# Performance work log

Measured on AMD Instinct MI355X. Metric: run time of the kernel, lower is better.

## Reference

```python
import jax, jax.numpy as jnp
import numpy as np
from jax import lax

B, T, D, H, L = 2048, 512, 64, 16, 10
LOG2PI = float(np.log(2.0 * np.pi))


def _gru_cell(x, h, Wih, Whh, bih, bhh):
    # torch GRUCell gate order: r, z, n
    gi = x @ Wih.T + bih
    gh = h @ Whh.T + bhh
    ir, iz, inn = jnp.split(gi, 3, axis=-1)
    hr, hz, hn = jnp.split(gh, 3, axis=-1)
    r = jax.nn.sigmoid(ir + hr)
    z = jax.nn.sigmoid(iz + hz)
    n = jnp.tanh(inn + r * hn)
    return (1.0 - z) * n + z * h


def _mlp_head(h, W1, b1, W2, b2, Wmu, bmu, Wcov, bcov):
    hh = jax.nn.relu(h @ W1.T + b1)
    hh = jax.nn.relu(hh @ W2.T + b2)
    mu = hh @ Wmu.T + bmu
    sigma = jnp.exp(hh @ Wcov.T + bcov)
    return mu, sigma


def setup_inputs():
    key = jax.random.key(0)
    ks = jax.random.split(key, 24)

    def he(k, shape, fan_in):
        return jax.random.normal(k, shape, dtype=jnp.float32) * np.float32(np.sqrt(2.0 / fan_in))

    z = lambda *s: jnp.zeros(s, jnp.float32)
    p = {}
    p['x'] = jax.random.normal(ks[0], (B, T, D), dtype=jnp.float32)
    p['eps'] = jax.random.normal(ks[1], (B, T, L), dtype=jnp.float32)
    # bidirectional inference GRU
    p['bi_Wih_f'] = he(ks[2], (3 * H, D), D); p['bi_Whh_f'] = he(ks[3], (3 * H, H), H)
    p['bi_bih_f'] = z(3 * H); p['bi_bhh_f'] = z(3 * H)
    p['bi_Wih_b'] = he(ks[4], (3 * H, D), D); p['bi_Whh_b'] = he(ks[5], (3 * H, H), H)
    p['bi_bih_b'] = z(3 * H); p['bi_bhh_b'] = z(3 * H)
    # inference GRUCell on [z_prev, context]
    p['infz_Wih'] = he(ks[6], (3 * H, L + 2 * H), L + 2 * H); p['infz_Whh'] = he(ks[7], (3 * H, H), H)
    p['infz_bih'] = z(3 * H); p['infz_bhh'] = z(3 * H)
    # inference MLP
    p['inf_W1'] = he(ks[8], (H, H), H); p['inf_b1'] = z(H)
    p['inf_W2'] = he(ks[9], (H, H), H); p['inf_b2'] = z(H)
    p['inf_Wmu'] = he(ks[10], (L, H), H); p['inf_bmu'] = z(L)
    p['inf_Wcov'] = he(ks[11], (L, H), H); p['inf_bcov'] = z(L)
    # generative prior GRUCell + MLP (frozen in torch)
    p['genz_Wih'] = he(ks[12], (3 * H, L), L); p['genz_Whh'] = he(ks[13], (3 * H, H), H)
    p['genz_bih'] = z(3 * H); p['genz_bhh'] = z(3 * H)
    p['genzmlp_W1'] = he(ks[14], (H, H), H); p['genzmlp_b1'] = z(H)
    p['genzmlp_W2'] = he(ks[15], (H, H), H); p['genzmlp_b2'] = z(H)
    p['genzmlp_Wmu'] = he(ks[16], (L, H), H); p['genzmlp_bmu'] = z(L)
    p['genzmlp_Wcov'] = he(ks[17], (L, H), H); p['genzmlp_bcov'] = z(L)
    # generative emission GRUCell + MLP (outputs 3*D)
    p['genr_Wih'] = he(ks[18], (3 * H, L), L); p['genr_Whh'] = he(ks[19], (3 * H, H), H)
    p['genr_bih'] = z(3 * H); p['genr_bhh'] = z(3 * H)
    p['genr_W1'] = he(ks[20], (H, H), H); p['genr_b1'] = z(H)
    p['genr_W2'] = he(ks[21], (3 * D, H), H); p['genr_b2'] = z(3 * D)
    return p


def _forward(x, eps, bi_Wih_f, bi_Whh_f, bi_bih_f, bi_bhh_f, bi_Wih_b, bi_Whh_b, bi_bih_b, bi_bhh_b,
             infz_Wih, infz_Whh, infz_bih, infz_bhh,
             inf_W1, inf_b1, inf_W2, inf_b2, inf_Wmu, inf_bmu, inf_Wcov, inf_bcov,
             genz_Wih, genz_Whh, genz_bih, genz_bhh,
             genzmlp_W1, genzmlp_b1, genzmlp_W2, genzmlp_b2, genzmlp_Wmu, genzmlp_bmu, genzmlp_Wcov, genzmlp_bcov,
             genr_Wih, genr_Whh, genr_bih, genr_bhh, genr_W1, genr_b1, genr_W2, genr_b2):
    b, t, d = x.shape
    xt = jnp.transpose(x, (1, 0, 2))      # [T, B, D] time-major
    eps_t = jnp.transpose(eps, (1, 0, 2))  # [T, B, L]
    h0 = jnp.zeros((b, H), x.dtype)

    def fstep(h, xin):
        h2 = _gru_cell(xin, h, bi_Wih_f, bi_Whh_f, bi_bih_f, bi_bhh_f)
        return h2, h2

    def bstep(h, xin):
        h2 = _gru_cell(xin, h, bi_Wih_b, bi_Whh_b, bi_bih_b, bi_bhh_b)
        return h2, h2

    _, fwd = lax.scan(fstep, h0, xt)               # [T, B, H]
    _, bwd_rev = lax.scan(bstep, h0, xt[::-1])
    bwd = bwd_rev[::-1]                            # [T, B, H]

    pad = jnp.zeros((1, b, H), x.dtype)
    h_right = jnp.concatenate([pad, fwd[:-1]], axis=0)   # h^{->}_{t-1}
    h_left = jnp.concatenate([bwd[1:], pad], axis=0)     # h^{<-}_{t+1}
    ctx = jnp.concatenate([h_right, h_left], axis=-1)    # [T, B, 2H]

    def step(carry, inp):
        h_z, h_gz, h_gr, z_prev = carry
        c, e, xi = inp
        h_z = _gru_cell(jnp.concatenate([z_prev, c], axis=-1), h_z, infz_Wih, infz_Whh, infz_bih, infz_bhh)
        q_mu, q_sig = _mlp_head(h_z, inf_W1, inf_b1, inf_W2, inf_b2, inf_Wmu, inf_bmu, inf_Wcov, inf_bcov)
        h_gz = _gru_cell(z_prev, h_gz, genz_Wih, genz_Whh, genz_bih, genz_bhh)
        p_mu, p_sig = _mlp_head(h_gz, genzmlp_W1, genzmlp_b1, genzmlp_W2, genzmlp_b2, genzmlp_Wmu, genzmlp_bmu, genzmlp_Wcov, genzmlp_bcov)
        # KL(N(q_mu,q_sig) || N(p_mu,p_sig))
        kl = jnp.log(p_sig / q_sig) + (q_sig * q_sig + (q_mu - p_mu) ** 2) / (2.0 * p_sig * p_sig) - 0.5
        kl_t = kl.sum(axis=-1).mean()
        z_t = q_mu + q_sig * e  # rsample
        h_gr = _gru_cell(z_t, h_gr, genr_Wih, genr_Whh, genr_bih, genr_bhh)
        r = jax.nn.relu(h_gr @ genr_W1.T + genr_b1) @ genr_W2.T + genr_b2  # [B, 3D]
        r_mu = r[:, :d]
        r_diag = jnp.exp(r[:, d:2 * d]) + 1e-4
        w = r[:, 2 * d:]  # rank-1 cov factor
        # LowRankMVN log_prob via Woodbury (rank 1): Cov = D + w w^T
        delta = xi - r_mu
        dinv = 1.0 / r_diag
        wd = w * dinv
        cap = 1.0 + jnp.sum(wd * w, axis=-1)  # capacitance
        maha = jnp.sum(delta * delta * dinv, axis=-1) - jnp.sum(wd * delta, axis=-1) ** 2 / cap
        logdet = jnp.sum(jnp.log(r_diag), axis=-1) + jnp.log(cap)
        logp = -0.5 * (d * LOG2PI + logdet + maha)
        nll_t = -logp.mean()
        return (h_z, h_gz, h_gr, z_t), (kl_t, nll_t)

    z0 = jnp.zeros((b, L), x.dtype)
    carry0 = (h0, h0, h0, z0)
    _, (kls, nlls) = lax.scan(step, carry0, (ctx, eps_t, xt))
    return nlls.sum(), kls.sum()


def reference(x, eps, bi_Wih_f, bi_Whh_f, bi_bih_f, bi_bhh_f, bi_Wih_b, bi_Whh_b, bi_bih_b, bi_bhh_b,
              infz_Wih, infz_Whh, infz_bih, infz_bhh,
              inf_W1, inf_b1, inf_W2, inf_b2, inf_Wmu, inf_bmu, inf_Wcov, inf_bcov,
              genz_Wih, genz_Whh, genz_bih, genz_bhh,
              genzmlp_W1, genzmlp_b1, genzmlp_W2, genzmlp_b2, genzmlp_Wmu, genzmlp_bmu, genzmlp_Wcov, genzmlp_bcov,
              genr_Wih, genr_Whh, genr_bih, genr_bhh, genr_W1, genr_b1, genr_W2, genr_b2):
    return _forward(x, eps, bi_Wih_f, bi_Whh_f, bi_bih_f, bi_bhh_f, bi_Wih_b, bi_Whh_b, bi_bih_b, bi_bhh_b,
                    infz_Wih, infz_Whh, infz_bih, infz_bhh,
                    inf_W1, inf_b1, inf_W2, inf_b2, inf_Wmu, inf_bmu, inf_Wcov, inf_bcov,
                    genz_Wih, genz_Whh, genz_bih, genz_bhh,
                    genzmlp_W1, genzmlp_b1, genzmlp_W2, genzmlp_b2, genzmlp_Wmu, genzmlp_bmu, genzmlp_Wcov, genzmlp_bcov,
                    genr_Wih, genr_Whh, genr_bih, genr_bhh, genr_W1, genr_b1, genr_W2, genr_b2)
```

## Files before the change

### kernel.cpp

```cpp
#include <hip/hip_runtime.h>

namespace {

typedef __attribute__((ext_vector_type(4))) _Float16 half4v;
typedef __attribute__((ext_vector_type(4))) float   float4v;
typedef unsigned int u32;

#define MFMA16(a,b,c) __builtin_amdgcn_mfma_f32_16x16x16f16((a),(b),(c),0,0,0)

constexpr int Bb = 2048;
constexpr int Tt = 512;
constexpr float LOG2PI_ = 1.8378770664093453f;

struct InPtrs { const float* p[42]; };

__device__ __forceinline__ float rcpf(float x){ return __builtin_amdgcn_rcpf(x); }
__device__ __forceinline__ float sigm(float x){ return rcpf(1.0f + __expf(-x)); }
__device__ __forceinline__ float tanh_(float x){ return 1.0f - 2.0f*rcpf(1.0f + __expf(2.0f*x)); }

__device__ __forceinline__ void barrier_lds(){
  asm volatile("s_waitcnt lgkmcnt(0)" ::: "memory");
  __builtin_amdgcn_s_barrier();
  asm volatile("" ::: "memory");
}

__global__ void zero2(float* out){ if (threadIdx.x < 2) out[threadIdx.x] = 0.f; }

__device__ __forceinline__ void gru_update(const float4v& Dr, const float4v& Dz,
                                           const float4v& Dn, const float4v& Dh, half4v& hB){
  #pragma unroll
  for (int i = 0; i < 4; ++i){
    const float rr = sigm(Dr[i]);
    const float zz = sigm(Dz[i]);
    const float nn = tanh_(Dn[i] + rr*Dh[i]);
    const float hp = (float)hB[i];
    hB[i] = (_Float16)((1.f - zz)*nn + zz*hp);
  }
}

__device__ __forceinline__ half4v relu_pack(const float4v& D){
  half4v o;
  #pragma unroll
  for (int i = 0; i < 4; ++i) o[i] = (_Float16)fmaxf(D[i], 0.f);
  return o;
}

constexpr int CH = 8;
constexpr int NCH = Tt / CH;

__global__ __launch_bounds__(128,1) void bigru(InPtrs ip, _Float16* __restrict__ hf,
                                               _Float16* __restrict__ hb)
{
  const int tid = threadIdx.x;
  const int w = tid >> 6;
  const int l = tid & 63, r = l & 15, q = l >> 4;
  const int dir = blockIdx.y;
  const int base = blockIdx.x * 16;

  const float* __restrict__ x   = ip.p[0];
  const float* __restrict__ Wih = dir ? ip.p[6] : ip.p[2];
  const float* __restrict__ Whh = dir ? ip.p[7] : ip.p[3];
  const float* __restrict__ bih = dir ? ip.p[8] : ip.p[4];
  const float* __restrict__ bhh = dir ? ip.p[9] : ip.p[5];
  _Float16* __restrict__ hout = dir ? hb : hf;

  __shared__ __align__(16) float giS[2][CH][64][12];

  half4v Wi[3][4];
  float  b0[4], b1[4], b2[4];
  float4v xp[CH][4];
  half4v Wh[3];
  float  bh2[4];
  half4v hB = {0,0,0,0};
  const float* xrow = x + (size_t)(base + r) * Tt * 64;

  if (w == 1){
    #pragma unroll
    for (int rt = 0; rt < 3; ++rt)
      #pragma unroll
      for (int kt = 0; kt < 4; ++kt)
        #pragma unroll
        for (int j = 0; j < 4; ++j)
          Wi[rt][kt][j] = (_Float16)Wih[(rt*16 + r)*64 + kt*16 + q*4 + j];
    #pragma unroll
    for (int i = 0; i < 4; ++i){
      const int row = q*4 + i;
      b0[i] = bih[row]      + bhh[row];
      b1[i] = bih[16 + row] + bhh[16 + row];
      b2[i] = bih[32 + row];
    }
    #pragma unroll
    for (int s = 0; s < CH; ++s){
      const int tn = dir ? Tt-1-s : s;
      #pragma unroll
      for (int kt = 0; kt < 4; ++kt)
        xp[s][kt] = *(const float4v*)(xrow + (size_t)tn*64 + kt*16 + q*4);
    }
  } else {
    #pragma unroll
    for (int rt = 0; rt < 3; ++rt)
      #pragma unroll
      for (int j = 0; j < 4; ++j)
        Wh[rt][j] = (_Float16)Whh[(rt*16 + r)*16 + q*4 + j];
    #pragma unroll
    for (int i = 0; i < 4; ++i) bh2[i] = bhh[32 + q*4 + i];
  }

  for (int c = 0; c < NCH; ++c){
    if (w == 1){
      #pragma unroll
      for (int st = 0; st < CH; ++st){
        const int tg = c*CH + st;
        half4v xB[4];
        #pragma unroll
        for (int kt = 0; kt < 4; ++kt)
          #pragma unroll
          for (int j = 0; j < 4; ++j) xB[kt][j] = (_Float16)xp[st][kt][j];
        const int tp = tg + CH;
        if (tp < Tt){
          const int tn = dir ? Tt-1-tp : tp;
          #pragma unroll
          for (int kt = 0; kt < 4; ++kt)
            xp[st][kt] = *(const float4v*)(xrow + (size_t)tn*64 + kt*16 + q*4);
        }
        float4v A0 = {b0[0],b0[1],b0[2],b0[3]};
        float4v A1 = {b1[0],b1[1],b1[2],b1[3]};
        float4v A2 = {b2[0],b2[1],b2[2],b2[3]};
        #pragma unroll
        for (int kt = 0; kt < 4; ++kt){
          A0 = MFMA16(Wi[0][kt], xB[kt], A0);
          A1 = MFMA16(Wi[1][kt], xB[kt], A1);
          A2 = MFMA16(Wi[2][kt], xB[kt], A2);
        }
        float* o = &giS[c&1][st][l][0];
        *(float4v*)(o + 0) = A0;
        *(float4v*)(o + 4) = A1;
        *(float4v*)(o + 8) = A2;
      }
    }
    barrier_lds();
    if (w == 0){
      for (int st = 0; st < CH; ++st){
        const int tg = c*CH + st;
        const int t = dir ? Tt-1-tg : tg;
        const float* gi = &giS[c&1][st][l][0];
        float4v A0 = *(const float4v*)(gi + 0);
        float4v A1 = *(const float4v*)(gi + 4);
        float4v A2 = *(const float4v*)(gi + 8);
        float4v Dh = {bh2[0],bh2[1],bh2[2],bh2[3]};
        A0 = MFMA16(Wh[0], hB, A0);
        A1 = MFMA16(Wh[1], hB, A1);
        Dh = MFMA16(Wh[2], hB, Dh);
        gru_update(A0, A1, A2, Dh, hB);
        *(half4v*)(hout + (((size_t)t*Bb + base + r) << 4) + q*4) = hB;
      }
    }
  }
}

__global__ __launch_bounds__(192,1) void vae_seq(InPtrs ip, const _Float16* __restrict__ hf,
                                                 const _Float16* __restrict__ hb,
                                                 _Float16* __restrict__ hz,
                                                 _Float16* __restrict__ hgz,
                                                 _Float16* __restrict__ hgr)
{
  const int tid = threadIdx.x;
  const int w = tid / 64;
  const int l = tid & 63, r = l & 15, q = l >> 4;
  const int base = blockIdx.x * 16;
  const int row0 = q*4;

  __shared__ u32 zS[3][2][64];
  for (int i = tid; i < 3*2*64; i += 192) ((u32*)zS)[i] = 0u;
  barrier_lds();

  half4v WizA[3][3], WhzA[3], I1A, I2A, IMuA, ICovA;
  float bz0[4], bz1[4], bzn[4], bzh[4], bI1v[4], bI2v[4], bIMu[4], bICov[4];
  half4v hzB = {0,0,0,0}, zB = {0,0,0,0};
  half4v hrN = {0,0,0,0}, hlN = {0,0,0,0};
  float eN[4];
  half4v WgzA[3], WhgzA[3];
  float bg0[4], bg1[4], bgn[4], bgh[4];
  half4v hgzB = {0,0,0,0};
  half4v WgrA[3], WhgrA[3];
  float br0[4], br1[4], brn[4], brh[4];
  half4v hgrB = {0,0,0,0};

  const float* erow = ip.p[1] + (size_t)(base + r) * Tt * 10;

  if (w == 0){
    #pragma unroll
    for (int rt = 0; rt < 3; ++rt)
      #pragma unroll
      for (int kt = 0; kt < 3; ++kt)
        #pragma unroll
        for (int j = 0; j < 4; ++j){
          const int k = kt*16 + q*4 + j;
          int c;
          if (kt == 0) c = (k < 10) ? k : -1;
          else if (kt == 1) c = 10 + (k - 16);
          else c = 26 + (k - 32);
          WizA[rt][kt][j] = (c >= 0) ? (_Float16)ip.p[10][(rt*16 + r)*42 + c] : (_Float16)0.f;
        }
    #pragma unroll
    for (int rt = 0; rt < 3; ++rt)
      #pragma unroll
      for (int j = 0; j < 4; ++j)
        WhzA[rt][j] = (_Float16)ip.p[11][(rt*16 + r)*16 + q*4 + j];
    #pragma unroll
    for (int j = 0; j < 4; ++j){
      const int k = q*4 + j;
      I1A[j]  = (_Float16)ip.p[14][r*16 + k];
      I2A[j]  = (_Float16)ip.p[16][r*16 + k];
      IMuA[j] = (r < 10) ? (_Float16)ip.p[18][r*16 + k] : (_Float16)0.f;
      ICovA[j]= (r < 10) ? (_Float16)ip.p[20][r*16 + k] : (_Float16)0.f;
    }
    #pragma unroll
    for (int i = 0; i < 4; ++i){
      const int row = row0 + i;
      bz0[i] = ip.p[12][row]    + ip.p[13][row];
      bz1[i] = ip.p[12][16+row] + ip.p[13][16+row];
      bzn[i] = ip.p[12][32+row];
      bzh[i] = ip.p[13][32+row];
      bI1v[i] = ip.p[15][row];  bI2v[i] = ip.p[17][row];
      bIMu[i]  = (row < 10) ? ip.p[19][row] : 0.f;
      bICov[i] = (row < 10) ? ip.p[21][row] : 0.f;
    }
    hlN = *(const half4v*)(hb + (((size_t)1*Bb + base + r) << 4) + q*4);
    #pragma unroll
    for (int i = 0; i < 4; ++i) eN[i] = (row0 + i < 10) ? erow[row0 + i] : 0.f;
  } else if (w == 1){
    #pragma unroll
    for (int rt = 0; rt < 3; ++rt)
      #pragma unroll
      for (int j = 0; j < 4; ++j){
        const int k = q*4 + j;
        WgzA[rt][j]  = (k < 10) ? (_Float16)ip.p[22][(rt*16 + r)*10 + k] : (_Float16)0.f;
        WhgzA[rt][j] = (_Float16)ip.p[23][(rt*16 + r)*16 + k];
      }
    #pragma unroll
    for (int i = 0; i < 4; ++i){
      const int row = row0 + i;
      bg0[i] = ip.p[24][row]    + ip.p[25][row];
      bg1[i] = ip.p[24][16+row] + ip.p[25][16+row];
      bgn[i] = ip.p[24][32+row];
      bgh[i] = ip.p[25][32+row];
    }
  } else {
    #pragma unroll
    for (int rt = 0; rt < 3; ++rt)
      #pragma unroll
      for (int j = 0; j < 4; ++j){
        const int k = q*4 + j;
        WgrA[rt][j]  = (k < 10) ? (_Float16)ip.p[34][(rt*16 + r)*10 + k] : (_Float16)0.f;
        WhgrA[rt][j] = (_Float16)ip.p[35][(rt*16 + r)*16 + k];
      }
    #pragma unroll
    for (int i = 0; i < 4; ++i){
      const int row = row0 + i;
      br0[i] = ip.p[36][row]    + ip.p[37][row];
      br1[i] = ip.p[36][16+row] + ip.p[37][16+row];
      brn[i] = ip.p[36][32+row];
      brh[i] = ip.p[37][32+row];
    }
  }

  for (int i = 0; i < Tt + 2; ++i){
    if (w == 0){
      if (i < Tt){
        const half4v hrB = hrN, hlB = hlN;
        float ev[4];
        #pragma unroll
        for (int ii = 0; ii < 4; ++ii) ev[ii] = eN[ii];
        if (i < Tt-1){
          const int tn = i + 1;
          hrN = *(const half4v*)(hf + (((size_t)(tn-1)*Bb + base + r) << 4) + q*4);
          if (tn < Tt-1) hlN = *(const half4v*)(hb + (((size_t)(tn+1)*Bb + base + r) << 4) + q*4);
          else { half4v zz0 = {0,0,0,0}; hlN = zz0; }
          #pragma unroll
          for (int ii = 0; ii < 4; ++ii) eN[ii] = (row0 + ii < 10) ? erow[tn*10 + row0 + ii] : 0.f;
        }
        float4v Dr = {bz0[0],bz0[1],bz0[2],bz0[3]};
        float4v Dz = {bz1[0],bz1[1],bz1[2],bz1[3]};
        float4v Dn = {bzn[0],bzn[1],bzn[2],bzn[3]};
        float4v Dh = {bzh[0],bzh[1],bzh[2],bzh[3]};
        Dr = MFMA16(WizA[0][0], zB, Dr); Dr = MFMA16(WizA[0][1], hrB, Dr); Dr = MFMA16(WizA[0][2], hlB, Dr);
        Dz = MFMA16(WizA[1][0], zB, Dz); Dz = MFMA16(WizA[1][1], hrB, Dz); Dz = MFMA16(WizA[1][2], hlB, Dz);
        Dn = MFMA16(WizA[2][0], zB, Dn); Dn = MFMA16(WizA[2][1], hrB, Dn); Dn = MFMA16(WizA[2][2], hlB, Dn);
        Dr = MFMA16(WhzA[0], hzB, Dr);
        Dz = MFMA16(WhzA[1], hzB, Dz);
        Dh = MFMA16(WhzA[2], hzB, Dh);
        gru_update(Dr, Dz, Dn, Dh, hzB);
        *(half4v*)(hz + (((size_t)i*Bb + base + r) << 4) + q*4) = hzB;

        float4v H1 = {bI1v[0],bI1v[1],bI1v[2],bI1v[3]};
        H1 = MFMA16(I1A, hzB, H1);
        const half4v h1B = relu_pack(H1);
        float4v H2 = {bI2v[0],bI2v[1],bI2v[2],bI2v[3]};
        H2 = MFMA16(I2A, h1B, H2);
        const half4v h2B = relu_pack(H2);
        float4v Qmu  = {bIMu[0],bIMu[1],bIMu[2],bIMu[3]};
        float4v Qpre = {bICov[0],bICov[1],bICov[2],bICov[3]};
        Qmu  = MFMA16(IMuA,  h2B, Qmu);
        Qpre = MFMA16(ICovA, h2B, Qpre);

        const int slot = i % 3;
        #pragma unroll
        for (int ii = 0; ii < 4; ++ii){
          const float qs = __expf(Qpre[ii]);
          zB[ii] = (_Float16)(Qmu[ii] + qs*ev[ii]);
        }
        union { half4v h; u32 u[2]; } zc; zc.h = zB;
        zS[slot][0][l] = zc.u[0];
        zS[slot][1][l] = zc.u[1];
      }
    } else if (w == 1){
      if (i >= 1 && i <= Tt){
        const int s = i - 1;
        const int sp = (s - 1 + 3) % 3;
        union { half4v h; u32 u[2]; } zc;
        zc.u[0] = zS[sp][0][l]; zc.u[1] = zS[sp][1][l];
        const half4v zPrev = zc.h;

        float4v Er = {bg0[0],bg0[1],bg0[2],bg0[3]};
        float4v Ez = {bg1[0],bg1[1],bg1[2],bg1[3]};
        float4v En = {bgn[0],bgn[1],bgn[2],bgn[3]};
        float4v Eh = {bgh[0],bgh[1],bgh[2],bgh[3]};
        Er = MFMA16(WgzA[0], zPrev, Er); Er = MFMA16(WhgzA[0], hgzB, Er);
        Ez = MFMA16(WgzA[1], zPrev, Ez); Ez = MFMA16(WhgzA[1], hgzB, Ez);
        En = MFMA16(WgzA[2], zPrev, En);
        Eh = MFMA16(WhgzA[2], hgzB, Eh);
        gru_update(Er, Ez, En, Eh, hgzB);
        *(half4v*)(hgz + (((size_t)s*Bb + base + r) << 4) + q*4) = hgzB;
      }
    } else {
      if (i >= 2){
        const int u = i - 2;
        union { half4v h; u32 uu[2]; } zc;
        zc.uu[0] = zS[u % 3][0][l]; zc.uu[1] = zS[u % 3][1][l];
        const half4v zU = zc.h;

        float4v Fr = {br0[0],br0[1],br0[2],br0[3]};
        float4v Fz = {br1[0],br1[1],br1[2],br1[3]};
        float4v Fn = {brn[0],brn[1],brn[2],brn[3]};
        float4v Fh = {brh[0],brh[1],brh[2],brh[3]};
        Fr = MFMA16(WgrA[0], zU, Fr); Fr = MFMA16(WhgrA[0], hgrB, Fr);
        Fz = MFMA16(WgrA[1], zU, Fz); Fz = MFMA16(WhgrA[1], hgrB, Fz);
        Fn = MFMA16(WgrA[2], zU, Fn);
        Fh = MFMA16(WhgrA[2], hgrB, Fh);
        gru_update(Fr, Fz, Fn, Fh, hgrB);
        *(half4v*)(hgr + (((size_t)u*Bb + base + r) << 4) + q*4) = hgrB;
      }
    }
    barrier_lds();
  }
}

__global__ __launch_bounds__(256,4) void kl_epi(InPtrs ip, const _Float16* __restrict__ hz,
                                                const _Float16* __restrict__ hgz,
                                                float* __restrict__ out)
{
  const int tid = threadIdx.x;
  const int l = tid & 63, r = l & 15, q = l >> 4;
  const int row0 = q*4;
  const int wid = blockIdx.x * 4 + (tid >> 6);
  const int u0 = wid * 16;

  half4v I1A, I2A, IMuA, ICovA, Z1A, Z2A, ZMuA, ZCovA;
  float bI1v[4], bI2v[4], bIMu[4], bICov[4], bZ1v[4], bZ2v[4], bZMu[4], bZCov[4];
  #pragma unroll
  for (int j = 0; j < 4; ++j){
    const int k = q*4 + j;
    I1A[j]  = (_Float16)ip.p[14][r*16 + k];
    I2A[j]  = (_Float16)ip.p[16][r*16 + k];
    IMuA[j] = (r < 10) ? (_Float16)ip.p[18][r*16 + k] : (_Float16)0.f;
    ICovA[j]= (r < 10) ? (_Float16)ip.p[20][r*16 + k] : (_Float16)0.f;
    Z1A[j]  = (_Float16)ip.p[26][r*16 + k];
    Z2A[j]  = (_Float16)ip.p[28][r*16 + k];
    ZMuA[j] = (r < 10) ? (_Float16)ip.p[30][r*16 + k] : (_Float16)0.f;
    ZCovA[j]= (r < 10) ? (_Float16)ip.p[32][r*16 + k] : (_Float16)0.f;
  }
  #pragma unroll
  for (int i = 0; i < 4; ++i){
    const int row = row0 + i;
    bI1v[i] = ip.p[15][row];  bI2v[i] = ip.p[17][row];
    bIMu[i]  = (row < 10) ? ip.p[19][row] : 0.f;
    bICov[i] = (row < 10) ? ip.p[21][row] : 0.f;
    bZ1v[i] = ip.p[27][row];  bZ2v[i] = ip.p[29][row];
    bZMu[i]  = (row < 10) ? ip.p[31][row] : 0.f;
    bZCov[i] = (row < 10) ? ip.p[33][row] : 0.f;
  }

  float kl_acc = 0.f;
  for (int k = 0; k < 16; ++k){
    const int u = u0 + k;
    const int tile = u >> 9, t = u & 511;
    const size_t off = (((size_t)t*Bb + tile*16 + r) << 4) + q*4;
    const half4v hzB  = *(const half4v*)(hz  + off);
    const half4v hgzB = *(const half4v*)(hgz + off);

    float4v H1 = {bI1v[0],bI1v[1],bI1v[2],bI1v[3]};
    H1 = MFMA16(I1A, hzB, H1);
    const half4v h1B = relu_pack(H1);
    float4v H2 = {bI2v[0],bI2v[1],bI2v[2],bI2v[3]};
    H2 = MFMA16(I2A, h1B, H2);
    const half4v h2B = relu_pack(H2);
    float4v Qmu  = {bIMu[0],bIMu[1],bIMu[2],bIMu[3]};
    float4v Qpre = {bICov[0],bICov[1],bICov[2],bICov[3]};
    Qmu  = MFMA16(IMuA,  h2B, Qmu);
    Qpre = MFMA16(ICovA, h2B, Qpre);

    float4v G1 = {bZ1v[0],bZ1v[1],bZ1v[2],bZ1v[3]};
    G1 = MFMA16(Z1A, hgzB, G1);
    const half4v g1B = relu_pack(G1);
    float4v G2 = {bZ2v[0],bZ2v[1],bZ2v[2],bZ2v[3]};
    G2 = MFMA16(Z2A, g1B, G2);
    const half4v g2B = relu_pack(G2);
    float4v Pmu  = {bZMu[0],bZMu[1],bZMu[2],bZMu[3]};
    float4v Ppre = {bZCov[0],bZCov[1],bZCov[2],bZCov[3]};
    Pmu  = MFMA16(ZMuA,  g2B, Pmu);
    Ppre = MFMA16(ZCovA, g2B, Ppre);

    #pragma unroll
    for (int ii = 0; ii < 4; ++ii){
      const float qs = __expf(Qpre[ii]);
      const float dm = Qmu[ii] - Pmu[ii];
      kl_acc += (Ppre[ii] - Qpre[ii]) + (qs*qs + dm*dm)*0.5f*__expf(-2.f*Ppre[ii]) - 0.5f;
    }
  }
  #pragma unroll
  for (int m = 1; m < 64; m <<= 1) kl_acc += __shfl_xor(kl_acc, m, 64);
  if (l == 0) atomicAdd(&out[1], kl_acc * (1.f/(float)Bb));
}

__global__ __launch_bounds__(256,2) void nll_epi(InPtrs ip, const _Float16* __restrict__ hgr,
                                                 float* __restrict__ out)
{
  const int tid = threadIdx.x;
  const int l = tid & 63, r = l & 15, q = l >> 4;
  const int row0 = q*4;
  const int wid = blockIdx.x * 4 + (tid >> 6);
  const int u0 = wid * 16;

  half4v R1A, R2A[12];
  float bR1v[4], bR2v[12][4];
  #pragma unroll
  for (int j = 0; j < 4; ++j){
    const int k = q*4 + j;
    R1A[j] = (_Float16)ip.p[38][r*16 + k];
    #pragma unroll
    for (int m = 0; m < 12; ++m)
      R2A[m][j] = (_Float16)ip.p[40][(m*16 + r)*16 + k];
  }
  #pragma unroll
  for (int i = 0; i < 4; ++i){
    const int row = row0 + i;
    bR1v[i] = ip.p[39][row];
    #pragma unroll
    for (int m = 0; m < 12; ++m) bR2v[m][i] = ip.p[41][m*16 + row];
  }

  float nll_acc = 0.f;
  for (int k = 0; k < 16; ++k){
    const int u = u0 + k;
    const int tile = u >> 9, t = u & 511;
    const half4v hgrB = *(const half4v*)(hgr + (((size_t)t*Bb + tile*16 + r) << 4) + q*4);
    const float* xrow = ip.p[0] + ((size_t)(tile*16 + r) * Tt + t) * 64;
    float4v xv[4];
    #pragma unroll
    for (int m = 0; m < 4; ++m) xv[m] = *(const float4v*)(xrow + m*16 + q*4);

    float4v R1D = {bR1v[0],bR1v[1],bR1v[2],bR1v[3]};
    R1D = MFMA16(R1A, hgrB, R1D);
    const half4v r1B = relu_pack(R1D);

    float s1 = 0.f, s2 = 0.f, s3 = 0.f, s4 = 0.f;
    #pragma unroll
    for (int m = 0; m < 4; ++m){
      float4v Dmu = {bR2v[m][0],bR2v[m][1],bR2v[m][2],bR2v[m][3]};
      float4v Ddp = {bR2v[4+m][0],bR2v[4+m][1],bR2v[4+m][2],bR2v[4+m][3]};
      float4v Dw  = {bR2v[8+m][0],bR2v[8+m][1],bR2v[8+m][2],bR2v[8+m][3]};
      Dmu = MFMA16(R2A[m],   r1B, Dmu);
      Ddp = MFMA16(R2A[4+m], r1B, Ddp);
      Dw  = MFMA16(R2A[8+m], r1B, Dw);
      #pragma unroll
      for (int ii = 0; ii < 4; ++ii){
        const float diag = __expf(Ddp[ii]) + 1e-4f;
        const float dinv = rcpf(diag);
        const float delta = xv[m][ii] - Dmu[ii];
        const float wv = Dw[ii];
        s1 += delta*delta*dinv;
        s2 += wv*wv*dinv;
        s3 += wv*dinv*delta;
        s4 += __logf(diag);
      }
    }
    s1 += __shfl_xor(s1, 16, 64); s1 += __shfl_xor(s1, 32, 64);
    s2 += __shfl_xor(s2, 16, 64); s2 += __shfl_xor(s2, 32, 64);
    s3 += __shfl_xor(s3, 16, 64); s3 += __shfl_xor(s3, 32, 64);
    s4 += __shfl_xor(s4, 16, 64); s4 += __shfl_xor(s4, 32, 64);
    const float cap = 1.f + s2;
    const float maha = s1 - s3*s3*rcpf(cap);
    const float logdet = s4 + __logf(cap);
    nll_acc += 0.5f*(64.f*LOG2PI_ + logdet + maha);
  }
  #pragma unroll
  for (int m = 1; m < 64; m <<= 1) nll_acc += __shfl_xor(nll_acc, m, 64);
  if (l == 0) atomicAdd(&out[0], nll_acc * 0.25f * (1.f/(float)Bb));
}

}

extern "C" void kernel_launch(void* const* d_in, const int* in_sizes, int n_in,
                              void* d_out, int out_size, void* d_ws, size_t ws_size,
                              hipStream_t stream)
{
  InPtrs ip;
  for (int i = 0; i < 42; ++i) ip.p[i] = (const float*)d_in[i];
  float* out = (float*)d_out;

  const size_t SZ = (size_t)Tt * Bb * 16;
  _Float16* hf  = (_Float16*)d_ws;
  _Float16* hb  = hf  + SZ;
  _Float16* hz  = hb  + SZ;
  _Float16* hgz = hz  + SZ;
  _Float16* hgr = hgz + SZ;

  zero2<<<1, 64, 0, stream>>>(out);
  dim3 gb(Bb/16, 2);
  bigru<<<gb, 128, 0, stream>>>(ip, hf, hb);
  vae_seq<<<Bb/16, 192, 0, stream>>>(ip, hf, hb, hz, hgz, hgr);
  kl_epi<<<1024, 256, 0, stream>>>(ip, hz, hgz, out);
  nll_epi<<<1024, 256, 0, stream>>>(ip, hgr, out);
}
```

Baseline: 1.067 ms.

## Deepen prefetch in VAE sequence loop, reorder MFMAs, merge epilogue kernels

In the serial VAE recurrence kernel, the next-step prefetch of the bi-GRU states and eps becomes a 4-deep register ring, and the loop is unrolled by four so global-load latency is hidden across several steps. The inference GRU MFMAs are reordered so the z-dependent products run last, shortening the critical path on the loop-carried dependency. The KL and NLL epilogue kernels are merged into one launch split by block index, and the GRU update is rewritten to save a multiply. These changes cost more registers in the sequential kernel, and the merged epilogue now runs at a lower occupancy bound for the KL half.

```diff
diff --git a/kernel.cpp b/kernel.cpp
--- a/kernel.cpp
+++ b/kernel.cpp
@@ -34,7 +34,7 @@
     const float zz = sigm(Dz[i]);
     const float nn = tanh_(Dn[i] + rr*Dh[i]);
     const float hp = (float)hB[i];
-    hB[i] = (_Float16)((1.f - zz)*nn + zz*hp);
+    hB[i] = (_Float16)(nn + zz*(hp - nn));
   }
 }
 
@@ -140,6 +140,7 @@
     }
     barrier_lds();
     if (w == 0){
+      #pragma unroll
       for (int st = 0; st < CH; ++st){
         const int tg = c*CH + st;
         const int t = dir ? Tt-1-tg : tg;
@@ -177,8 +178,8 @@
   half4v WizA[3][3], WhzA[3], I1A, I2A, IMuA, ICovA;
   float bz0[4], bz1[4], bzn[4], bzh[4], bI1v[4], bI2v[4], bIMu[4], bICov[4];
   half4v hzB = {0,0,0,0}, zB = {0,0,0,0};
-  half4v hrN = {0,0,0,0}, hlN = {0,0,0,0};
-  float eN[4];
+  half4v hrR[4], hlR[4];
+  float4v eR[4];
   half4v WgzA[3], WhgzA[3];
   float bg0[4], bg1[4], bgn[4], bgh[4];
   half4v hgzB = {0,0,0,0};
@@ -226,9 +227,16 @@
       bIMu[i]  = (row < 10) ? ip.p[19][row] : 0.f;
       bICov[i] = (row < 10) ? ip.p[21][row] : 0.f;
     }
-    hlN = *(const half4v*)(hb + (((size_t)1*Bb + base + r) << 4) + q*4);
-    #pragma unroll
-    for (int i = 0; i < 4; ++i) eN[i] = (row0 + i < 10) ? erow[row0 + i] : 0.f;
+    #pragma unroll
+    for (int s = 0; s < 4; ++s){
+      if (s >= 1) hrR[s] = *(const half4v*)(hf + (((size_t)(s-1)*Bb + base + r) << 4) + q*4);
+      else { half4v z0 = {0,0,0,0}; hrR[s] = z0; }
+      hlR[s] = *(const half4v*)(hb + (((size_t)(s+1)*Bb + base + r) << 4) + q*4);
+      float4v et;
+      #pragma unroll
+      for (int ii = 0; ii < 4; ++ii) et[ii] = (row0 + ii < 10) ? erow[s*10 + row0 + ii] : 0.f;
+      eR[s] = et;
+    }
   } else if (w == 1){
     #pragma unroll
     for (int rt = 0; rt < 3; ++rt)
@@ -265,248 +273,252 @@
     }
   }
 
-  for (int i = 0; i < Tt + 2; ++i){
-    if (w == 0){
-      if (i < Tt){
-        const half4v hrB = hrN, hlB = hlN;
-        float ev[4];
-        #pragma unroll
-        for (int ii = 0; ii < 4; ++ii) ev[ii] = eN[ii];
-        if (i < Tt-1){
-          const int tn = i + 1;
-          hrN = *(const half4v*)(hf + (((size_t)(tn-1)*Bb + base + r) << 4) + q*4);
-          if (tn < Tt-1) hlN = *(const half4v*)(hb + (((size_t)(tn+1)*Bb + base + r) << 4) + q*4);
-          else { half4v zz0 = {0,0,0,0}; hlN = zz0; }
+  for (int ib = 0; ib < Tt + 4; ib += 4){
+    #pragma unroll
+    for (int k = 0; k < 4; ++k){
+      const int i = ib + k;
+      if (w == 0){
+        if (i < Tt){
+          const half4v hrB = hrR[k], hlB = hlR[k];
+          const float4v ev = eR[k];
+          const int f = i + 4;
+          if (f < Tt){
+            hrR[k] = *(const half4v*)(hf + (((size_t)(f-1)*Bb + base + r) << 4) + q*4);
+            if (f <= Tt-2) hlR[k] = *(const half4v*)(hb + (((size_t)(f+1)*Bb + base + r) << 4) + q*4);
+            else { half4v z0 = {0,0,0,0}; hlR[k] = z0; }
+            float4v et;
+            #pragma unroll
+            for (int ii = 0; ii < 4; ++ii) et[ii] = (row0 + ii < 10) ? erow[f*10 + row0 + ii] : 0.f;
+            eR[k] = et;
+          }
+          float4v Dr = {bz0[0],bz0[1],bz0[2],bz0[3]};
+          float4v Dz = {bz1[0],bz1[1],bz1[2],bz1[3]};
+          float4v Dn = {bzn[0],bzn[1],bzn[2],bzn[3]};
+          float4v Dh = {bzh[0],bzh[1],bzh[2],bzh[3]};
+          Dr = MFMA16(WizA[0][1], hrB, Dr); Dr = MFMA16(WizA[0][2], hlB, Dr);
+          Dz = MFMA16(WizA[1][1], hrB, Dz); Dz = MFMA16(WizA[1][2], hlB, Dz);
+          Dn = MFMA16(WizA[2][1], hrB, Dn); Dn = MFMA16(WizA[2][2], hlB, Dn);
+          Dr = MFMA16(WhzA[0], hzB, Dr);
+          Dz = MFMA16(WhzA[1], hzB, Dz);
+          Dh = MFMA16(WhzA[2], hzB, Dh);
+          Dr = MFMA16(WizA[0][0], zB, Dr);
+          Dz = MFMA16(WizA[1][0], zB, Dz);
+          Dn = MFMA16(WizA[2][0], zB, Dn);
+          gru_update(Dr, Dz, Dn, Dh, hzB);
+          *(half4v*)(hz + (((size_t)i*Bb + base + r) << 4) + q*4) = hzB;
+
+          float4v H1 = {bI1v[0],bI1v[1],bI1v[2],bI1v[3]};
+          H1 = MFMA16(I1A, hzB, H1);
+          const half4v h1B = relu_pack(H1);
+          float4v H2 = {bI2v[0],bI2v[1],bI2v[2],bI2v[3]};
+          H2 = MFMA16(I2A, h1B, H2);
+          const half4v h2B = relu_pack(H2);
+          float4v Qmu  = {bIMu[0],bIMu[1],bIMu[2],bIMu[3]};
+          float4v Qpre = {bICov[0],bICov[1],bICov[2],bICov[3]};
+          Qmu  = MFMA16(IMuA,  h2B, Qmu);
+          Qpre = MFMA16(ICovA, h2B, Qpre);
+
+          const int slot = i % 3;
           #pragma unroll
-          for (int ii = 0; ii < 4; ++ii) eN[ii] = (row0 + ii < 10) ? erow[tn*10 + row0 + ii] : 0.f;
-        }
-        float4v Dr = {bz0[0],bz0[1],bz0[2],bz0[3]};
-        float4v Dz = {bz1[0],bz1[1],bz1[2],bz1[3]};
-        float4v Dn = {bzn[0],bzn[1],bzn[2],bzn[3]};
-        float4v Dh = {bzh[0],bzh[1],bzh[2],bzh[3]};
-        Dr = MFMA16(WizA[0][0], zB, Dr); Dr = MFMA16(WizA[0][1], hrB, Dr); Dr = MFMA16(WizA[0][2], hlB, Dr);
-        Dz = MFMA16(WizA[1][0], zB, Dz); Dz = MFMA16(WizA[1][1], hrB, Dz); Dz = MFMA16(WizA[1][2], hlB, Dz);
-        Dn = MFMA16(WizA[2][0], zB, Dn); Dn = MFMA16(WizA[2][1], hrB, Dn); Dn = MFMA16(WizA[2][2], hlB, Dn);
-        Dr = MFMA16(WhzA[0], hzB, Dr);
-        Dz = MFMA16(WhzA[1], hzB, Dz);
-        Dh = MFMA16(WhzA[2], hzB, Dh);
-        gru_update(Dr, Dz, Dn, Dh, hzB);
-        *(half4v*)(hz + (((size_t)i*Bb + base + r) << 4) + q*4) = hzB;
-
-        float4v H1 = {bI1v[0],bI1v[1],bI1v[2],bI1v[3]};
-        H1 = MFMA16(I1A, hzB, H1);
-        const half4v h1B = relu_pack(H1);
-        float4v H2 = {bI2v[0],bI2v[1],bI2v[2],bI2v[3]};
-        H2 = MFMA16(I2A, h1B, H2);
-        const half4v h2B = relu_pack(H2);
-        float4v Qmu  = {bIMu[0],bIMu[1],bIMu[2],bIMu[3]};
-        float4v Qpre = {bICov[0],bICov[1],bICov[2],bICov[3]};
-        Qmu  = MFMA16(IMuA,  h2B, Qmu);
-        Qpre = MFMA16(ICovA, h2B, Qpre);
-
-        const int slot = i % 3;
-        #pragma unroll
-        for (int ii = 0; ii < 4; ++ii){
-          const float qs = __expf(Qpre[ii]);
-          zB[ii] = (_Float16)(Qmu[ii] + qs*ev[ii]);
-        }
-        union { half4v h; u32 u[2]; } zc; zc.h = zB;
-        zS[slot][0][l] = zc.u[0];
-        zS[slot][1][l] = zc.u[1];
-      }
-    } else if (w == 1){
-      if (i >= 1 && i <= Tt){
-        const int s = i - 1;
-        const int sp = (s - 1 + 3) % 3;
-        union { half4v h; u32 u[2]; } zc;
-        zc.u[0] = zS[sp][0][l]; zc.u[1] = zS[sp][1][l];
-        const half4v zPrev = zc.h;
-
-        float4v Er = {bg0[0],bg0[1],bg0[2],bg0[3]};
-        float4v Ez = {bg1[0],bg1[1],bg1[2],bg1[3]};
-        float4v En = {bgn[0],bgn[1],bgn[2],bgn[3]};
-        float4v Eh = {bgh[0],bgh[1],bgh[2],bgh[3]};
-        Er = MFMA16(WgzA[0], zPrev, Er); Er = MFMA16(WhgzA[0], hgzB, Er);
-        Ez = MFMA16(WgzA[1], zPrev, Ez); Ez = MFMA16(WhgzA[1], hgzB, Ez);
-        En = MFMA16(WgzA[2], zPrev, En);
-        Eh = MFMA16(WhgzA[2], hgzB, Eh);
-        gru_update(Er, Ez, En, Eh, hgzB);
-        *(half4v*)(hgz + (((size_t)s*Bb + base + r) << 4) + q*4) = hgzB;
-      }
-    } else {
-      if (i >= 2){
-        const int u = i - 2;
-        union { half4v h; u32 uu[2]; } zc;
-        zc.uu[0] = zS[u % 3][0][l]; zc.uu[1] = zS[u % 3][1][l];
-        const half4v zU = zc.h;
-
-        float4v Fr = {br0[0],br0[1],br0[2],br0[3]};
-        float4v Fz = {br1[0],br1[1],br1[2],br1[3]};
-        float4v Fn = {brn[0],brn[1],brn[2],brn[3]};
-        float4v Fh = {brh[0],brh[1],brh[2],brh[3]};
-        Fr = MFMA16(WgrA[0], zU, Fr); Fr = MFMA16(WhgrA[0], hgrB, Fr);
-        Fz = MFMA16(WgrA[1], zU, Fz); Fz = MFMA16(WhgrA[1], hgrB, Fz);
-        Fn = MFMA16(WgrA[2], zU, Fn);
-        Fh = MFMA16(WhgrA[2], hgrB, Fh);
-        gru_update(Fr, Fz, Fn, Fh, hgrB);
-        *(half4v*)(hgr + (((size_t)u*Bb + base + r) << 4) + q*4) = hgrB;
-      }
-    }
-    barrier_lds();
+          for (int ii = 0; ii < 4; ++ii){
+            const float qs = __expf(Qpre[ii]);
+            zB[ii] = (_Float16)(Qmu[ii] + qs*ev[ii]);
+          }
+          union { half4v h; u32 u[2]; } zc; zc.h = zB;
+          zS[slot][0][l] = zc.u[0];
+          zS[slot][1][l] = zc.u[1];
+        }
+      } else if (w == 1){
+        if (i >= 1 && i <= Tt){
+          const int s = i - 1;
+          const int sp = (s - 1 + 3) % 3;
+          union { half4v h; u32 u[2]; } zc;
+          zc.u[0] = zS[sp][0][l]; zc.u[1] = zS[sp][1][l];
+          const half4v zPrev = zc.h;
+
+          float4v Er = {bg0[0],bg0[1],bg0[2],bg0[3]};
+          float4v Ez = {bg1[0],bg1[1],bg1[2],bg1[3]};
+          float4v En = {bgn[0],bgn[1],bgn[2],bgn[3]};
+          float4v Eh = {bgh[0],bgh[1],bgh[2],bgh[3]};
+          Er = MFMA16(WgzA[0], zPrev, Er); Er = MFMA16(WhgzA[0], hgzB, Er);
+          Ez = MFMA16(WgzA[1], zPrev, Ez); Ez = MFMA16(WhgzA[1], hgzB, Ez);
+          En = MFMA16(WgzA[2], zPrev, En);
+          Eh = MFMA16(WhgzA[2], hgzB, Eh);
+          gru_update(Er, Ez, En, Eh, hgzB);
+          *(half4v*)(hgz + (((size_t)s*Bb + base + r) << 4) + q*4) = hgzB;
+        }
+      } else {
+        if (i >= 2 && i < Tt + 2){
+          const int u = i - 2;
+          union { half4v h; u32 uu[2]; } zc;
+          zc.uu[0] = zS[u % 3][0][l]; zc.uu[1] = zS[u % 3][1][l];
+          const half4v zU = zc.h;
+
+          float4v Fr = {br0[0],br0[1],br0[2],br0[3]};
+          float4v Fz = {br1[0],br1[1],br1[2],br1[3]};
+          float4v Fn = {brn[0],brn[1],brn[2],brn[3]};
+          float4v Fh = {brh[0],brh[1],brh[2],brh[3]};
+          Fr = MFMA16(WgrA[0], zU, Fr); Fr = MFMA16(WhgrA[0], hgrB, Fr);
+          Fz = MFMA16(WgrA[1], zU, Fz); Fz = MFMA16(WhgrA[1], hgrB, Fz);
+          Fn = MFMA16(WgrA[2], zU, Fn);
+          Fh = MFMA16(WhgrA[2], hgrB, Fh);
+          gru_update(Fr, Fz, Fn, Fh, hgrB);
+          *(half4v*)(hgr + (((size_t)u*Bb + base + r) << 4) + q*4) = hgrB;
+        }
+      }
+      barrier_lds();
+    }
   }
 }
 
-__global__ __launch_bounds__(256,4) void kl_epi(InPtrs ip, const _Float16* __restrict__ hz,
-                                                const _Float16* __restrict__ hgz,
-                                                float* __restrict__ out)
+__global__ __launch_bounds__(256,2) void epi(InPtrs ip, const _Float16* __restrict__ hz,
+                                             const _Float16* __restrict__ hgz,
+                                             const _Float16* __restrict__ hgr,
+                                             float* __restrict__ out)
 {
   const int tid = threadIdx.x;
   const int l = tid & 63, r = l & 15, q = l >> 4;
   const int row0 = q*4;
-  const int wid = blockIdx.x * 4 + (tid >> 6);
-  const int u0 = wid * 16;
-
-  half4v I1A, I2A, IMuA, ICovA, Z1A, Z2A, ZMuA, ZCovA;
-  float bI1v[4], bI2v[4], bIMu[4], bICov[4], bZ1v[4], bZ2v[4], bZMu[4], bZCov[4];
-  #pragma unroll
-  for (int j = 0; j < 4; ++j){
-    const int k = q*4 + j;
-    I1A[j]  = (_Float16)ip.p[14][r*16 + k];
-    I2A[j]  = (_Float16)ip.p[16][r*16 + k];
-    IMuA[j] = (r < 10) ? (_Float16)ip.p[18][r*16 + k] : (_Float16)0.f;
-    ICovA[j]= (r < 10) ? (_Float16)ip.p[20][r*16 + k] : (_Float16)0.f;
-    Z1A[j]  = (_Float16)ip.p[26][r*16 + k];
-    Z2A[j]  = (_Float16)ip.p[28][r*16 + k];
-    ZMuA[j] = (r < 10) ? (_Float16)ip.p[30][r*16 + k] : (_Float16)0.f;
-    ZCovA[j]= (r < 10) ? (_Float16)ip.p[32][r*16 + k] : (_Float16)0.f;
+
+  if (blockIdx.x < 1024){
+    const int wid = blockIdx.x * 4 + (tid >> 6);
+    const int u0 = wid * 16;
+
+    half4v I1A, I2A, IMuA, ICovA, Z1A, Z2A, ZMuA, ZCovA;
+    float bI1v[4], bI2v[4], bIMu[4], bICov[4], bZ1v[4], bZ2v[4], bZMu[4], bZCov[4];
+    #pragma unroll
+    for (int j = 0; j < 4; ++j){
+      const int k = q*4 + j;
+      I1A[j]  = (_Float16)ip.p[14][r*16 + k];
+      I2A[j]  = (_Float16)ip.p[16][r*16 + k];
+      IMuA[j] = (r < 10) ? (_Float16)ip.p[18][r*16 + k] : (_Float16)0.f;
+      ICovA[j]= (r < 10) ? (_Float16)ip.p[20][r*16 + k] : (_Float16)0.f;
+      Z1A[j]  = (_Float16)ip.p[26][r*16 + k];
+      Z2A[j]  = (_Float16)ip.p[28][r*16 + k];
+      ZMuA[j] = (r < 10) ? (_Float16)ip.p[30][r*16 + k] : (_Float16)0.f;
+      ZCovA[j]= (r < 10) ? (_Float16)ip.p[32][r*16 + k] : (_Float16)0.f;
+    }
+    #pragma unroll
+    for (int i = 0; i < 4; ++i){
+      const int row = row0 + i;
+      bI1v[i] = ip.p[15][row];  bI2v[i] = ip.p[17][row];
+      bIMu[i]  = (row < 10) ? ip.p[19][row] : 0.f;
+      bICov[i] = (row < 10) ? ip.p[21][row] : 0.f;
+      bZ1v[i] = ip.p[27][row];  bZ2v[i] = ip.p[29][row];
+      bZMu[i]  = (row < 10) ? ip.p[31][row] : 0.f;
+      bZCov[i] = (row < 10) ? ip.p[33][row] : 0.f;
+    }
+
+    float kl_acc = 0.f;
+    for (int k = 0; k < 16; ++k){
+      const int u = u0 + k;
+      const int tile = u >> 9, t = u & 511;
+      const size_t off = (((size_t)t*Bb + tile*16 + r) << 4) + q*4;
+      const half4v hzB  = *(const half4v*)(hz  + off);
+      const half4v hgzB = *(const half4v*)(hgz + off);
+
+      float4v H1 = {bI1v[0],bI1v[1],bI1v[2],bI1v[3]};
+      H1 = MFMA16(I1A, hzB, H1);
+      const half4v h1B = relu_pack(H1);
+      float4v H2 = {bI2v[0],bI2v[1],bI2v[2],bI2v[3]};
+      H2 = MFMA16(I2A, h1B, H2);
+      const half4v h2B = relu_pack(H2);
+      float4v Qmu  = {bIMu[0],bIMu[1],bIMu[2],bIMu[3]};
+      float4v Qpre = {bICov[0],bICov[1],bICov[2],bICov[3]};
+      Qmu  = MFMA16(IMuA,  h2B, Qmu);
+      Qpre = MFMA16(ICovA, h2B, Qpre);
+
+      float4v G1 = {bZ1v[0],bZ1v[1],bZ1v[2],bZ1v[3]};
+      G1 = MFMA16(Z1A, hgzB, G1);
+      const half4v g1B = relu_pack(G1);
+      float4v G2 = {bZ2v[0],bZ2v[1],bZ2v[2],bZ2v[3]};
+      G2 = MFMA16(Z2A, g1B, G2);
+      const half4v g2B = relu_pack(G2);
+      float4v Pmu  = {bZMu[0],bZMu[1],bZMu[2],bZMu[3]};
+      float4v Ppre = {bZCov[0],bZCov[1],bZCov[2],bZCov[3]};
+      Pmu  = MFMA16(ZMuA,  g2B, Pmu);
+      Ppre = MFMA16(ZCovA, g2B, Ppre);
+
+      #pragma unroll
+      for (int ii = 0; ii < 4; ++ii){
+        const float qs = __expf(Qpre[ii]);
+        const float dm = Qmu[ii] - Pmu[ii];
+        kl_acc += (Ppre[ii] - Qpre[ii]) + (qs*qs + dm*dm)*0.5f*__expf(-2.f*Ppre[ii]) - 0.5f;
+      }
+    }
+    #pragma unroll
+    for (int m = 1; m < 64; m <<= 1) kl_acc += __shfl_xor(kl_acc, m, 64);
+    if (l == 0) atomicAdd(&out[1], kl_acc * (1.f/(float)Bb));
+  } else {
+    const int wid = (blockIdx.x - 1024) * 4 + (tid >> 6);
+    const int u0 = wid * 16;
+
+    half4v R1A, R2A[12];
+    float bR1v[4], bR2v[12][4];
+    #pragma unroll
+    for (int j = 0; j < 4; ++j){
+      const int k = q*4 + j;
+      R1A[j] = (_Float16)ip.p[38][r*16 + k];
+      #pragma unroll
+      for (int m = 0; m < 12; ++m)
+        R2A[m][j] = (_Float16)ip.p[40][(m*16 + r)*16 + k];
+    }
+    #pragma unroll
+    for (int i = 0; i < 4; ++i){
+      const int row = row0 + i;
+      bR1v[i] = ip.p[39][row];
+      #pragma unroll
+      for (int m = 0; m < 12; ++m) bR2v[m][i] = ip.p[41][m*16 + row];
+    }
+
+    float nll_acc = 0.f;
+    for (int k = 0; k < 16; ++k){
+      const int u = u0 + k;
+      const int tile = u >> 9, t = u & 511;
+      const half4v hgrB = *(const half4v*)(hgr + (((size_t)t*Bb + tile*16 + r) << 4) + q*4);
+      const float* xrow = ip.p[0] + ((size_t)(tile*16 + r) * Tt + t) * 64;
+      float4v xv[4];
+      #pragma unroll
+      for (int m = 0; m < 4; ++m) xv[m] = *(const float4v*)(xrow + m*16 + q*4);
+
+      float4v R1D = {bR1v[0],bR1v[1],bR1v[2],bR1v[3]};
+      R1D = MFMA16(R1A, hgrB, R1D);
+      const half4v r1B = relu_pack(R1D);
+
+      float s1 = 0.f, s2 = 0.f, s3 = 0.f, s4 = 0.f;
+      #pragma unroll
+      for (int m = 0; m < 4; ++m){
+        float4v Dmu = {bR2v[m][0],bR2v[m][1],bR2v[m][2],bR2v[m][3]};
+        float4v Ddp = {bR2v[4+m][0],bR2v[4+m][1],bR2v[4+m][2],bR2v[4+m][3]};
+        float4v Dw  = {bR2v[8+m][0],bR2v[8+m][1],bR2v[8+m][2],bR2v[8+m][3]};
+        Dmu = MFMA16(R2A[m],   r1B, Dmu);
+        Ddp = MFMA16(R2A[4+m], r1B, Ddp);
+        Dw  = MFMA16(R2A[8+m], r1B, Dw);
+        #pragma unroll
+        for (int ii = 0; ii < 4; ++ii){
+          const float diag = __expf(Ddp[ii]) + 1e-4f;
+          const float dinv = rcpf(diag);
+          const float delta = xv[m][ii] - Dmu[ii];
+          const float wv = Dw[ii];
+          s1 += delta*delta*dinv;
+          s2 += wv*wv*dinv;
+          s3 += wv*dinv*delta;
+          s4 += __logf(diag);
+        }
+      }
+      s1 += __shfl_xor(s1, 16, 64); s1 += __shfl_xor(s1, 32, 64);
+      s2 += __shfl_xor(s2, 16, 64); s2 += __shfl_xor(s2, 32, 64);
+      s3 += __shfl_xor(s3, 16, 64); s3 += __shfl_xor(s3, 32, 64);
+      s4 += __shfl_xor(s4, 16, 64); s4 += __shfl_xor(s4, 32, 64);
+      const float cap = 1.f + s2;
+      const float maha = s1 - s3*s3*rcpf(cap);
+      const float logdet = s4 + __logf(cap);
+      nll_acc += 0.5f*(64.f*LOG2PI_ + logdet + maha);
+    }
+    #pragma unroll
+    for (int m = 1; m < 64; m <<= 1) nll_acc += __shfl_xor(nll_acc, m, 64);
+    if (l == 0) atomicAdd(&out[0], nll_acc * 0.25f * (1.f/(float)Bb));
   }
-  #pragma unroll
-  for (int i = 0; i < 4; ++i){
-    const int row = row0 + i;
-    bI1v[i] = ip.p[15][row];  bI2v[i] = ip.p[17][row];
-    bIMu[i]  = (row < 10) ? ip.p[19][row] : 0.f;
-    bICov[i] = (row < 10) ? ip.p[21][row] : 0.f;
-    bZ1v[i] = ip.p[27][row];  bZ2v[i] = ip.p[29][row];
-    bZMu[i]  = (row < 10) ? ip.p[31][row] : 0.f;
-    bZCov[i] = (row < 10) ? ip.p[33][row] : 0.f;
-  }
-
-  float kl_acc = 0.f;
-  for (int k = 0; k < 16; ++k){
-    const int u = u0 + k;
-    const int tile = u >> 9, t = u & 511;
-    const size_t off = (((size_t)t*Bb + tile*16 + r) << 4) + q*4;
-    const half4v hzB  = *(const half4v*)(hz  + off);
-    const half4v hgzB = *(const half4v*)(hgz + off);
-
-    float4v H1 = {bI1v[0],bI1v[1],bI1v[2],bI1v[3]};
-    H1 = MFMA16(I1A, hzB, H1);
-    const half4v h1B = relu_pack(H1);
-    float4v H2 = {bI2v[0],bI2v[1],bI2v[2],bI2v[3]};
-    H2 = MFMA16(I2A, h1B, H2);
-    const half4v h2B = relu_pack(H2);
-    float4v Qmu  = {bIMu[0],bIMu[1],bIMu[2],bIMu[3]};
-    float4v Qpre = {bICov[0],bICov[1],bICov[2],bICov[3]};
-    Qmu  = MFMA16(IMuA,  h2B, Qmu);
-    Qpre = MFMA16(ICovA, h2B, Qpre);
-
-    float4v G1 = {bZ1v[0],bZ1v[1],bZ1v[2],bZ1v[3]};
-    G1 = MFMA16(Z1A, hgzB, G1);
-    const half4v g1B = relu_pack(G1);
-    float4v G2 = {bZ2v[0],bZ2v[1],bZ2v[2],bZ2v[3]};
-    G2 = MFMA16(Z2A, g1B, G2);
-    const half4v g2B = relu_pack(G2);
-    float4v Pmu  = {bZMu[0],bZMu[1],bZMu[2],bZMu[3]};
-    float4v Ppre = {bZCov[0],bZCov[1],bZCov[2],bZCov[3]};
-    Pmu  = MFMA16(ZMuA,  g2B, Pmu);
-    Ppre = MFMA16(ZCovA, g2B, Ppre);
-
-    #pragma unroll
-    for (int ii = 0; ii < 4; ++ii){
-      const float qs = __expf(Qpre[ii]);
-      const float dm = Qmu[ii] - Pmu[ii];
-      kl_acc += (Ppre[ii] - Qpre[ii]) + (qs*qs + dm*dm)*0.5f*__expf(-2.f*Ppre[ii]) - 0.5f;
-    }
-  }
-  #pragma unroll
-  for (int m = 1; m < 64; m <<= 1) kl_acc += __shfl_xor(kl_acc, m, 64);
-  if (l == 0) atomicAdd(&out[1], kl_acc * (1.f/(float)Bb));
-}
-
-__global__ __launch_bounds__(256,2) void nll_epi(InPtrs ip, const _Float16* __restrict__ hgr,
-                                                 float* __restrict__ out)
-{
-  const int tid = threadIdx.x;
-  const int l = tid & 63, r = l & 15, q = l >> 4;
-  const int row0 = q*4;
-  const int wid = blockIdx.x * 4 + (tid >> 6);
-  const int u0 = wid * 16;
-
-  half4v R1A, R2A[12];
-  float bR1v[4], bR2v[12][4];
-  #pragma unroll
-  for (int j = 0; j < 4; ++j){
-    const int k = q*4 + j;
-    R1A[j] = (_Float16)ip.p[38][r*16 + k];
-    #pragma unroll
-    for (int m = 0; m < 12; ++m)
-      R2A[m][j] = (_Float16)ip.p[40][(m*16 + r)*16 + k];
-  }
-  #pragma unroll
-  for (int i = 0; i < 4; ++i){
-    const int row = row0 + i;
-    bR1v[i] = ip.p[39][row];
-    #pragma unroll
-    for (int m = 0; m < 12; ++m) bR2v[m][i] = ip.p[41][m*16 + row];
-  }
-
-  float nll_acc = 0.f;
-  for (int k = 0; k < 16; ++k){
-    const int u = u0 + k;
-    const int tile = u >> 9, t = u & 511;
-    const half4v hgrB = *(const half4v*)(hgr + (((size_t)t*Bb + tile*16 + r) << 4) + q*4);
-    const float* xrow = ip.p[0] + ((size_t)(tile*16 + r) * Tt + t) * 64;
-    float4v xv[4];
-    #pragma unroll
-    for (int m = 0; m < 4; ++m) xv[m] = *(const float4v*)(xrow + m*16 + q*4);
-
-    float4v R1D = {bR1v[0],bR1v[1],bR1v[2],bR1v[3]};
-    R1D = MFMA16(R1A, hgrB, R1D);
-    const half4v r1B = relu_pack(R1D);
-
-    float s1 = 0.f, s2 = 0.f, s3 = 0.f, s4 = 0.f;
-    #pragma unroll
-    for (int m = 0; m < 4; ++m){
-      float4v Dmu = {bR2v[m][0],bR2v[m][1],bR2v[m][2],bR2v[m][3]};
-      float4v Ddp = {bR2v[4+m][0],bR2v[4+m][1],bR2v[4+m][2],bR2v[4+m][3]};
-      float4v Dw  = {bR2v[8+m][0],bR2v[8+m][1],bR2v[8+m][2],bR2v[8+m][3]};
-      Dmu = MFMA16(R2A[m],   r1B, Dmu);
-      Ddp = MFMA16(R2A[4+m], r1B, Ddp);
-      Dw  = MFMA16(R2A[8+m], r1B, Dw);
-      #pragma unroll
-      for (int ii = 0; ii < 4; ++ii){
-        const float diag = __expf(Ddp[ii]) + 1e-4f;
-        const float dinv = rcpf(diag);
-        const float delta = xv[m][ii] - Dmu[ii];
-        const float wv = Dw[ii];
-        s1 += delta*delta*dinv;
-        s2 += wv*wv*dinv;
-        s3 += wv*dinv*delta;
-        s4 += __logf(diag);
-      }
-    }
-    s1 += __shfl_xor(s1, 16, 64); s1 += __shfl_xor(s1, 32, 64);
-    s2 += __shfl_xor(s2, 16, 64); s2 += __shfl_xor(s2, 32, 64);
-    s3 += __shfl_xor(s3, 16, 64); s3 += __shfl_xor(s3, 32, 64);
-    s4 += __shfl_xor(s4, 16, 64); s4 += __shfl_xor(s4, 32, 64);
-    const float cap = 1.f + s2;
-    const float maha = s1 - s3*s3*rcpf(cap);
-    const float logdet = s4 + __logf(cap);
-    nll_acc += 0.5f*(64.f*LOG2PI_ + logdet + maha);
-  }
-  #pragma unroll
-  for (int m = 1; m < 64; m <<= 1) nll_acc += __shfl_xor(nll_acc, m, 64);
-  if (l == 0) atomicAdd(&out[0], nll_acc * 0.25f * (1.f/(float)Bb));
 }
 
 }
@@ -530,6 +542,5 @@
   dim3 gb(Bb/16, 2);
   bigru<<<gb, 128, 0, stream>>>(ip, hf, hb);
   vae_seq<<<Bb/16, 192, 0, stream>>>(ip, hf, hb, hz, hgz, hgr);
-  kl_epi<<<1024, 256, 0, stream>>>(ip, hz, hgz, out);
-  nll_epi<<<1024, 256, 0, stream>>>(ip, hgr, out);
-}
+  epi<<<2048, 256, 0, stream>>>(ip, hz, hgz, hgr, out);
+}
```

Result: faster. 1.029 ms (-3.5%).
